# Kernel tuning notes

Measured on AMD Instinct MI355X. Metric: run time of the kernel, lower is better.

The kernel has to match this reference:

```python
import jax, jax.numpy as jnp
import numpy as np

N, DEG, F_IN, F_OUT, H = 8192, 16, 1024, 128, 8


def setup_inputs() -> dict:
    key = jax.random.key(0)
    ks = jax.random.split(key, 6)
    features = jax.random.normal(ks[0], (N, F_IN), dtype=jnp.float32)
    adj = jax.random.randint(ks[1], (N, DEG), 0, N)  # fixed-degree adjacency
    W = jax.random.normal(ks[2], (H, F_IN, F_OUT), dtype=jnp.float32) / np.sqrt(F_IN)
    bW = jax.random.normal(ks[3], (H, F_OUT), dtype=jnp.float32) * 0.01
    a = jax.random.normal(ks[4], (H, 2 * F_OUT), dtype=jnp.float32) / np.sqrt(2.0 * F_OUT)
    ba = jax.random.normal(ks[5], (H,), dtype=jnp.float32) * 0.01
    return {"features": features, "adj": adj, "W": W, "bW": bW, "a": a, "ba": ba}


def reference(features, adj, W, bW, a, ba):
    n = features.shape[0]
    # neighbors with self appended last (matches adjlist[node] + [node])
    nbr = jnp.concatenate([adj, jnp.arange(n)[:, None]], axis=1)  # [N, DEG+1]
    # per-head linear transform: h[k] = features @ W_k + b_k
    h = jnp.einsum('nf,hfo->hno', features, W) + bW[:, None, :]  # [H, N, F_OUT]
    # attention score a_k([h_dst, h_src]) + bias decomposed into dst/src parts
    a_dst, a_src = a[:, :F_OUT], a[:, F_OUT:]
    s_dst = jnp.einsum('hno,ho->hn', h, a_dst)  # [H, N]
    s_src = jnp.einsum('hno,ho->hn', h, a_src)  # [H, N]
    scores = s_dst[:, :, None] + s_src[:, nbr] + ba[:, None, None]  # [H, N, DEG+1]
    scores = jax.nn.leaky_relu(scores, 0.2)
    alpha = jax.nn.softmax(scores, axis=-1)  # softmax over neighbors (incl. self)
    h_src = h[:, nbr]  # [H, N, DEG+1, F_OUT]
    out = jnp.einsum('hnd,hndf->hnf', alpha, h_src)  # [H, N, F_OUT]
    # concat heads along feature dim -> [N, H*F_OUT]
    return out.transpose(1, 0, 2).reshape(n, H * F_OUT)
```

## Files before the change

### kernel.cpp

```cpp
#include <hip/hip_runtime.h>
#include <hip/hip_bf16.h>

#define N_NODES 8192
#define DEG     16
#define F_IN    1024
#define F_OUT   128
#define NH      8

typedef __bf16 bf16x8 __attribute__((ext_vector_type(8)));
typedef float  f32x4  __attribute__((ext_vector_type(4)));

__device__ __forceinline__ float bf2f(unsigned short u) {
    union { unsigned int i; float f; } v;
    v.i = ((unsigned int)u) << 16;
    return v.f;
}
__device__ __forceinline__ unsigned short f2bf(float f) {
    union { float f; unsigned int u; } v; v.f = f;
    unsigned int u = v.u + 0x7FFFu + ((v.u >> 16) & 1u);
    return (unsigned short)(u >> 16);
}
__device__ __forceinline__ int detect_bf16(const unsigned int* __restrict__ w) {
    int hits = 0;
#pragma unroll
    for (int i = 0; i < 64; ++i) {
        unsigned int x = w[i * 131 + 17];
        int e = (x >> 7) & 0xFF;
        hits += (e >= 100 && e <= 140) ? 1 : 0;
    }
    return hits > 32;
}
__device__ __forceinline__ float rd_scalar(const void* p, int idx, int isbf) {
    return isbf ? bf2f(((const unsigned short*)p)[idx]) : ((const float*)p)[idx];
}
__device__ __forceinline__ void gload16(const void* g, void* l) {
    __builtin_amdgcn_global_load_lds(
        (const __attribute__((address_space(1))) void*)g,
        (__attribute__((address_space(3))) void*)l, 16, 0, 0);
}

__global__ __launch_bounds__(256) void prep_inputs(
    const void* __restrict__ feat, const void* __restrict__ W,
    unsigned short* __restrict__ featb, unsigned short* __restrict__ Wt)
{
    const int isbf = detect_bf16((const unsigned int*)feat);
    if (blockIdx.x < 4096) {
        size_t i8 = ((size_t)blockIdx.x * 256 + threadIdx.x) * 8;
        if (isbf) {
            *(uint4*)(featb + i8) = ((const uint4*)feat)[i8 / 8];
        } else {
            const float* s = (const float*)feat + i8;
            float4 u0 = *(const float4*)s;
            float4 u1 = *(const float4*)(s + 4);
            unsigned short t[8] = { f2bf(u0.x), f2bf(u0.y), f2bf(u0.z), f2bf(u0.w),
                                    f2bf(u1.x), f2bf(u1.y), f2bf(u1.z), f2bf(u1.w) };
            *(uint4*)(featb + i8) = *(const uint4*)t;
        }
    } else {
        __shared__ float tile[64][65];
        const int bx = blockIdx.x - 4096;
        const int h  = bx >> 5;
        const int kt = (bx >> 1) & 15;
        const int ot = bx & 1;
        const int t  = threadIdx.x;
#pragma unroll
        for (int i = 0; i < 16; ++i) {
            int id = i * 256 + t, r = id >> 6, c = id & 63;
            tile[r][c] = rd_scalar(W, ((h * 1024 + kt * 64 + r) * 128) + ot * 64 + c, isbf);
        }
        __syncthreads();
#pragma unroll
        for (int i = 0; i < 16; ++i) {
            int id = i * 256 + t, oc = id >> 6, kc = id & 63;
            Wt[(size_t)(h * 128 + ot * 64 + oc) * 1024 + kt * 64 + kc] = f2bf(tile[kc][oc]);
        }
    }
}

__global__ __launch_bounds__(256) void gat_gemm3(
    const unsigned short* __restrict__ featb,
    const unsigned short* __restrict__ Wt,
    const void* __restrict__ raw_feat,
    const void* __restrict__ bW, const void* __restrict__ a,
    const void* __restrict__ ba,
    __hip_bfloat16* __restrict__ hbuf,
    float* __restrict__ sdst, float* __restrict__ ssrc)
{
    const int rawbf = detect_bf16((const unsigned int*)raw_feat);

    const int h   = blockIdx.y;
    const int bxp = ((blockIdx.x & 7) << 3) | (blockIdx.x >> 3);
    const int n0  = bxp * 128;
    const int tid = threadIdx.x;

    __shared__ __align__(16) unsigned short As[2][128 * 64];
    __shared__ __align__(16) unsigned short Bs[2][128 * 64];

    const int lane = tid & 63;
    const int wave = tid >> 6;
    const int quad = lane >> 4;
    const int l16  = lane & 15;
    const int sw   = l16 & 7;

    f32x4 acc[2][8];
#pragma unroll
    for (int i = 0; i < 2; ++i)
#pragma unroll
        for (int j = 0; j < 8; ++j) acc[i][j] = (f32x4)0.f;

    const unsigned short* wbase = Wt + (size_t)h * F_OUT * F_IN;

    for (int k0 = 0; k0 < F_IN; k0 += 128) {
#pragma unroll
        for (int p = 0; p < 2; ++p) {
            const int kk0 = k0 + p * 64;
#pragma unroll
            for (int t = 0; t < 4; ++t) {
                const int r0  = t * 32 + wave * 8;
                const int row = r0 + (lane >> 3);
                const int gc  = (lane & 7) ^ (row & 7);
                gload16(&featb[(size_t)(n0 + row) * F_IN + kk0 + gc * 8],
                        &As[p][r0 * 64]);
                gload16(&wbase[(size_t)row * F_IN + kk0 + gc * 8],
                        &Bs[p][r0 * 64]);
            }
        }
        __syncthreads();

#pragma unroll
        for (int p = 0; p < 2; ++p) {
#pragma unroll
            for (int ks = 0; ks < 2; ++ks) {
                const int kc = ks * 4 + quad;
                const int cs = (kc ^ sw) * 8;
                bf16x8 af[2], bfr[8];
#pragma unroll
                for (int rt = 0; rt < 2; ++rt)
                    af[rt] = *(const bf16x8*)&As[p][(wave * 32 + rt * 16 + l16) * 64 + cs];
#pragma unroll
                for (int ct = 0; ct < 8; ++ct)
                    bfr[ct] = *(const bf16x8*)&Bs[p][(ct * 16 + l16) * 64 + cs];
#pragma unroll
                for (int rt = 0; rt < 2; ++rt)
#pragma unroll
                    for (int ct = 0; ct < 8; ++ct)
                        acc[rt][ct] = __builtin_amdgcn_mfma_f32_16x16x32_bf16(
                            af[rt], bfr[ct], acc[rt][ct], 0, 0, 0);
            }
        }
        __syncthreads();
    }

#pragma unroll
    for (int ct = 0; ct < 8; ++ct) {
        const int col = ct * 16 + l16;
        const float bwv = rd_scalar(bW, h * F_OUT + col, rawbf);
#pragma unroll
        for (int rt = 0; rt < 2; ++rt) {
            const int nrow = n0 + wave * 32 + rt * 16 + quad * 4;
            __hip_bfloat16* dst = hbuf + ((size_t)h * N_NODES + nrow) * F_OUT + col;
#pragma unroll
            for (int r = 0; r < 4; ++r)
                dst[(size_t)r * F_OUT] = __float2bfloat16(acc[rt][ct][r] + bwv);
        }
    }

    float adst[8], asrc[8];
#pragma unroll
    for (int ct = 0; ct < 8; ++ct) {
        const int col = ct * 16 + l16;
        adst[ct] = rd_scalar(a, h * 256 + col, rawbf);
        asrc[ct] = rd_scalar(a, h * 256 + 128 + col, rawbf);
    }
    float pd[2][4] = {}, ps[2][4] = {};
#pragma unroll
    for (int rt = 0; rt < 2; ++rt)
#pragma unroll
        for (int ct = 0; ct < 8; ++ct)
#pragma unroll
            for (int r = 0; r < 4; ++r) {
                pd[rt][r] += acc[rt][ct][r] * adst[ct];
                ps[rt][r] += acc[rt][ct][r] * asrc[ct];
            }
#pragma unroll
    for (int off = 1; off < 16; off <<= 1)
#pragma unroll
        for (int rt = 0; rt < 2; ++rt)
#pragma unroll
            for (int r = 0; r < 4; ++r) {
                pd[rt][r] += __shfl_xor(pd[rt][r], off, 64);
                ps[rt][r] += __shfl_xor(ps[rt][r], off, 64);
            }
    if (l16 == 0) {
        const float bav = rd_scalar(ba, h, rawbf);
#pragma unroll
        for (int rt = 0; rt < 2; ++rt) {
            const int base = n0 + wave * 32 + rt * 16 + quad * 4;
            float4 vd = { pd[rt][0] + bav, pd[rt][1] + bav,
                          pd[rt][2] + bav, pd[rt][3] + bav };
            float4 vs = { ps[rt][0], ps[rt][1], ps[rt][2], ps[rt][3] };
            *(float4*)&sdst[h * N_NODES + base] = vd;
            *(float4*)&ssrc[h * N_NODES + base] = vs;
        }
    }
}

__global__ __launch_bounds__(256) void gat_aggr4(
    const unsigned short* __restrict__ hbuf,
    const int* __restrict__ adj,
    const float* __restrict__ sdst, const float* __restrict__ ssrc,
    const void* __restrict__ raw_feat, void* __restrict__ out)
{
    const int isbf = detect_bf16((const unsigned int*)raw_feat);
    const int h    = blockIdx.x;
    const int wave = threadIdx.x >> 6;
    const int lane = threadIdx.x & 63;
    const int half = lane >> 5;
    const int l32  = lane & 31;
    const int n    = blockIdx.y * 8 + wave * 2 + half;

    int nbr = n;
    if (l32 < DEG) nbr = adj[n * DEG + l32];

    float s = -1e30f;
    if (l32 < 17) {
        float sv = sdst[h * N_NODES + n] + ssrc[h * N_NODES + nbr];
        s = sv > 0.f ? sv : 0.2f * sv;
    }
    float m = s;
#pragma unroll
    for (int off = 1; off < 32; off <<= 1)
        m = fmaxf(m, __shfl_xor(m, off, 64));
    float ev = (l32 < 17) ? __expf(s - m) : 0.f;
    float sum = ev;
#pragma unroll
    for (int off = 1; off < 32; off <<= 1)
        sum += __shfl_xor(sum, off, 64);
    ev *= (1.f / sum);

    const unsigned short* hb = hbuf + (size_t)h * N_NODES * F_OUT;
    const int fc    = l32 * 4;
    const int sbase = half << 5;
    float a0 = 0.f, a1 = 0.f, a2 = 0.f, a3 = 0.f;
#pragma unroll
    for (int d = 0; d < 17; ++d) {
        const int   nb = __shfl(nbr, sbase + d, 64);
        const float av = __shfl(ev,  sbase + d, 64);
        uint2 pk = *(const uint2*)&hb[(size_t)nb * F_OUT + fc];
        a0 += av * bf2f((unsigned short)(pk.x & 0xffffu));
        a1 += av * bf2f((unsigned short)(pk.x >> 16));
        a2 += av * bf2f((unsigned short)(pk.y & 0xffffu));
        a3 += av * bf2f((unsigned short)(pk.y >> 16));
    }

    const size_t oidx = (size_t)n * (NH * F_OUT) + h * F_OUT + fc;
    if (isbf) {
        uint2 res;
        res.x = (unsigned int)f2bf(a0) | ((unsigned int)f2bf(a1) << 16);
        res.y = (unsigned int)f2bf(a2) | ((unsigned int)f2bf(a3) << 16);
        *(uint2*)&((unsigned short*)out)[oidx] = res;
    } else {
        float4 res = { a0, a1, a2, a3 };
        *(float4*)&((float*)out)[oidx] = res;
    }
}

__global__ __launch_bounds__(256) void gat_gemm_fb(
    const void* __restrict__ feat, const void* __restrict__ W,
    const void* __restrict__ bW, __hip_bfloat16* __restrict__ hbuf)
{
    const int isbf = detect_bf16((const unsigned int*)feat);
    const int h = blockIdx.y, n0 = blockIdx.x * 128, tid = threadIdx.x;
    __shared__ __align__(16) unsigned short As[128][72];
    __shared__ __align__(16) unsigned short Bs[128][72];
    const int lane = tid & 63, wave = tid >> 6, quad = lane >> 4, l16 = lane & 15;
    f32x4 acc[2][8];
#pragma unroll
    for (int i = 0; i < 2; ++i)
#pragma unroll
        for (int j = 0; j < 8; ++j) acc[i][j] = (f32x4)0.f;
    for (int k0 = 0; k0 < F_IN; k0 += 64) {
        if (isbf) {
            const unsigned short* fbase = (const unsigned short*)feat + (size_t)n0 * F_IN;
            const unsigned short* wsrc  = (const unsigned short*)W +
                                          (size_t)h * F_IN * F_OUT + (size_t)k0 * F_OUT;
#pragma unroll
            for (int t = 0; t < 4; ++t) {
                int c = t * 256 + tid, row = c >> 3, kc = c & 7;
                *(uint4*)&As[row][kc * 8] = *(const uint4*)&fbase[row * F_IN + k0 + kc * 8];
            }
#pragma unroll
            for (int t = 0; t < 2; ++t) {
                int c = t * 256 + tid, kr2 = c >> 4, mm = c & 15, oc = mm * 8;
                uint4 w0 = *(const uint4*)&wsrc[(2 * kr2) * F_OUT + oc];
                uint4 w1 = *(const uint4*)&wsrc[(2 * kr2 + 1) * F_OUT + oc];
                const unsigned short* p0 = (const unsigned short*)&w0;
                const unsigned short* p1 = (const unsigned short*)&w1;
#pragma unroll
                for (int j = 0; j < 8; ++j) {
                    int i = (j + mm) & 7;
                    *(unsigned int*)&Bs[oc + i][2 * kr2] =
                        (unsigned int)p0[i] | ((unsigned int)p1[i] << 16);
                }
            }
        } else {
            const float* fbase = (const float*)feat + (size_t)n0 * F_IN;
            const float* wsrc  = (const float*)W +
                                 (size_t)h * F_IN * F_OUT + (size_t)k0 * F_OUT;
#pragma unroll
            for (int t = 0; t < 4; ++t) {
                int c = t * 256 + tid, row = c >> 3, kc = c & 7;
                const float* src = &fbase[row * F_IN + k0 + kc * 8];
                float4 u0 = *(const float4*)src, u1 = *(const float4*)(src + 4);
                unsigned short sh[8] = { f2bf(u0.x), f2bf(u0.y), f2bf(u0.z), f2bf(u0.w),
                                         f2bf(u1.x), f2bf(u1.y), f2bf(u1.z), f2bf(u1.w) };
                *(uint4*)&As[row][kc * 8] = *(const uint4*)sh;
            }
#pragma unroll
            for (int t = 0; t < 2; ++t) {
                int c = t * 256 + tid, kr2 = c >> 4, mm = c & 15, oc = mm * 8;
                const float* r0 = &wsrc[(2 * kr2) * F_OUT + oc];
                const float* r1 = &wsrc[(2 * kr2 + 1) * F_OUT + oc];
                float4 e0 = *(const float4*)r0, e1 = *(const float4*)(r0 + 4);
                float4 o0 = *(const float4*)r1, o1 = *(const float4*)(r1 + 4);
                unsigned short p0[8] = { f2bf(e0.x), f2bf(e0.y), f2bf(e0.z), f2bf(e0.w),
                                         f2bf(e1.x), f2bf(e1.y), f2bf(e1.z), f2bf(e1.w) };
                unsigned short p1[8] = { f2bf(o0.x), f2bf(o0.y), f2bf(o0.z), f2bf(o0.w),
                                         f2bf(o1.x), f2bf(o1.y), f2bf(o1.z), f2bf(o1.w) };
#pragma unroll
                for (int j = 0; j < 8; ++j) {
                    int i = (j + mm) & 7;
                    *(unsigned int*)&Bs[oc + i][2 * kr2] =
                        (unsigned int)p0[i] | ((unsigned int)p1[i] << 16);
                }
            }
        }
        __syncthreads();
#pragma unroll
        for (int ks = 0; ks < 2; ++ks) {
            const int kk = ks * 32 + quad * 8;
            bf16x8 af[2], bfr[8];
#pragma unroll
            for (int rt = 0; rt < 2; ++rt)
                af[rt] = *(const bf16x8*)&As[wave * 32 + rt * 16 + l16][kk];
#pragma unroll
            for (int ct = 0; ct < 8; ++ct)
                bfr[ct] = *(const bf16x8*)&Bs[ct * 16 + l16][kk];
#pragma unroll
            for (int rt = 0; rt < 2; ++rt)
#pragma unroll
                for (int ct = 0; ct < 8; ++ct)
                    acc[rt][ct] = __builtin_amdgcn_mfma_f32_16x16x32_bf16(
                        af[rt], bfr[ct], acc[rt][ct], 0, 0, 0);
        }
        __syncthreads();
    }
#pragma unroll
    for (int ct = 0; ct < 8; ++ct) {
        const int col = ct * 16 + l16;
        const float bwv = rd_scalar(bW, h * F_OUT + col, isbf);
#pragma unroll
        for (int rt = 0; rt < 2; ++rt) {
            const int nrow = n0 + wave * 32 + rt * 16 + quad * 4;
            __hip_bfloat16* dst = hbuf + ((size_t)h * N_NODES + nrow) * F_OUT + col;
#pragma unroll
            for (int r = 0; r < 4; ++r)
                dst[(size_t)r * F_OUT] = __float2bfloat16(acc[rt][ct][r] + bwv);
        }
    }
}

__global__ __launch_bounds__(256) void gat_aggr_fb(
    const __hip_bfloat16* __restrict__ hbuf, const int* __restrict__ adj,
    const void* __restrict__ a, const void* __restrict__ ba,
    void* __restrict__ out, const void* __restrict__ feat)
{
    const int isbf = detect_bf16((const unsigned int*)feat);
    const int n = blockIdx.x, wave = threadIdx.x >> 6, lane = threadIdx.x & 63;
    const int hh = blockIdx.y * 4 + wave;
    int nbr_reg = n;
    if (lane < DEG) nbr_reg = adj[n * DEG + lane];
    const int f0 = lane * 2;
    const float adst0 = rd_scalar(a, hh * 256 + f0, isbf);
    const float adst1 = rd_scalar(a, hh * 256 + f0 + 1, isbf);
    const float asrc0 = rd_scalar(a, hh * 256 + 128 + f0, isbf);
    const float asrc1 = rd_scalar(a, hh * 256 + 128 + f0 + 1, isbf);
    const float bav   = rd_scalar(ba, hh, isbf);
    const __hip_bfloat16* hb = hbuf + (size_t)hh * N_NODES * F_OUT;
    float v0[17], v1[17], red[18];
#pragma unroll
    for (int d = 0; d < 17; ++d) {
        int nb = __shfl(nbr_reg, d, 64);
        unsigned int pk = *(const unsigned int*)&hb[(size_t)nb * F_OUT + f0];
        v0[d] = bf2f((unsigned short)(pk & 0xffffu));
        v1[d] = bf2f((unsigned short)(pk >> 16));
        red[d] = v0[d] * asrc0 + v1[d] * asrc1;
    }
    red[17] = v0[16] * adst0 + v1[16] * adst1;
#pragma unroll
    for (int off = 1; off < 64; off <<= 1)
#pragma unroll
        for (int r = 0; r < 18; ++r) red[r] += __shfl_xor(red[r], off, 64);
    const float sd = red[17] + bav;
    float sc[17], mx = -1e30f;
#pragma unroll
    for (int d = 0; d < 17; ++d) {
        float s = sd + red[d];
        s = s > 0.f ? s : 0.2f * s;
        sc[d] = s; mx = fmaxf(mx, s);
    }
    float ssum = 0.f;
#pragma unroll
    for (int d = 0; d < 17; ++d) { sc[d] = __expf(sc[d] - mx); ssum += sc[d]; }
    const float inv = 1.f / ssum;
    float o0 = 0.f, o1 = 0.f;
#pragma unroll
    for (int d = 0; d < 17; ++d) { o0 += sc[d] * v0[d]; o1 += sc[d] * v1[d]; }
    o0 *= inv; o1 *= inv;
    const size_t oidx = (size_t)n * (NH * F_OUT) + hh * F_OUT + f0;
    if (isbf) {
        *(unsigned int*)&((unsigned short*)out)[oidx] =
            (unsigned int)f2bf(o0) | ((unsigned int)f2bf(o1) << 16);
    } else {
        float2 res; res.x = o0; res.y = o1;
        *(float2*)&((float*)out)[oidx] = res;
    }
}

extern "C" void kernel_launch(void* const* d_in, const int* in_sizes, int n_in,
                              void* d_out, int out_size, void* d_ws, size_t ws_size,
                              hipStream_t stream)
{
    const void* feat = d_in[0];
    const int*  adj  = (const int*)d_in[1];
    const void* W    = d_in[2];
    const void* bW   = d_in[3];
    const void* a    = d_in[4];
    const void* ba   = d_in[5];

    char* ws = (char*)d_ws;
    __hip_bfloat16* hbuf = (__hip_bfloat16*)ws;
    const size_t HB = (size_t)NH * N_NODES * F_OUT * 2;
    const size_t SC = (size_t)NH * N_NODES * 4;
    float* sdst = (float*)(ws + HB);
    float* ssrc = (float*)(ws + HB + SC);
    unsigned short* featb = (unsigned short*)(ws + HB + 2 * SC);
    unsigned short* Wt    = featb + (size_t)N_NODES * F_IN;
    const size_t needA = HB + 2 * SC +
        ((size_t)N_NODES * F_IN + (size_t)NH * F_IN * F_OUT) * 2;

    if (ws_size >= needA) {
        prep_inputs<<<4352, 256, 0, stream>>>(feat, W, featb, Wt);
        gat_gemm3<<<dim3(64, 8), 256, 0, stream>>>(featb, Wt, feat, bW, a, ba,
                                                   hbuf, sdst, ssrc);
        gat_aggr4<<<dim3(8, 1024), 256, 0, stream>>>((const unsigned short*)hbuf,
                                                     adj, sdst, ssrc, feat, d_out);
    } else {
        gat_gemm_fb<<<dim3(64, 8), 256, 0, stream>>>(feat, W, bW, hbuf);
        gat_aggr_fb<<<dim3(8192, 2), 256, 0, stream>>>(hbuf, adj, a, ba, d_out, feat);
    }
}
```

Baseline: 148.7 us.

## Split GEMM block across 8 waves in a 4x2 grid with LDS score reduction

The projection GEMM now runs with 512 threads per block, arranged as a 4x2 wave grid, so each wave computes a 32x64 output subtile instead of 32x128. This halves the accumulator registers per wave and doubles the waves available to hide latency, with each wave issuing fewer global loads per stage. Because the attention-score dot products are now split across two column waves, the partial sums are combined through shared memory, which adds a block barrier. The cost is more LDS fragment reads per MFMA, since the A fragments are loaded by two waves, and a little extra synchronisation.

```diff
diff --git a/kernel.cpp b/kernel.cpp
--- a/kernel.cpp
+++ b/kernel.cpp
@@ -77,7 +77,7 @@
     }
 }
 
-__global__ __launch_bounds__(256) void gat_gemm3(
+__global__ __launch_bounds__(512, 4) void gat_gemm6(
     const unsigned short* __restrict__ featb,
     const unsigned short* __restrict__ Wt,
     const void* __restrict__ raw_feat,
@@ -98,15 +98,19 @@
 
     const int lane = tid & 63;
     const int wave = tid >> 6;
+    const int wr   = wave >> 1;
+    const int wc   = wave & 1;
     const int quad = lane >> 4;
     const int l16  = lane & 15;
     const int sw   = l16 & 7;
-
-    f32x4 acc[2][8];
+    const int srow   = lane >> 3;
+    const int schunk = lane & 7;
+
+    f32x4 acc[2][4];
 #pragma unroll
     for (int i = 0; i < 2; ++i)
 #pragma unroll
-        for (int j = 0; j < 8; ++j) acc[i][j] = (f32x4)0.f;
+        for (int j = 0; j < 4; ++j) acc[i][j] = (f32x4)0.f;
 
     const unsigned short* wbase = Wt + (size_t)h * F_OUT * F_IN;
 
@@ -115,10 +119,10 @@
         for (int p = 0; p < 2; ++p) {
             const int kk0 = k0 + p * 64;
 #pragma unroll
-            for (int t = 0; t < 4; ++t) {
-                const int r0  = t * 32 + wave * 8;
-                const int row = r0 + (lane >> 3);
-                const int gc  = (lane & 7) ^ (row & 7);
+            for (int t = 0; t < 2; ++t) {
+                const int r0  = t * 64 + wave * 8;
+                const int row = r0 + srow;
+                const int gc  = schunk ^ (row & 7);
                 gload16(&featb[(size_t)(n0 + row) * F_IN + kk0 + gc * 8],
                         &As[p][r0 * 64]);
                 gload16(&wbase[(size_t)row * F_IN + kk0 + gc * 8],
@@ -133,17 +137,17 @@
             for (int ks = 0; ks < 2; ++ks) {
                 const int kc = ks * 4 + quad;
                 const int cs = (kc ^ sw) * 8;
-                bf16x8 af[2], bfr[8];
+                bf16x8 af[2], bfr[4];
 #pragma unroll
                 for (int rt = 0; rt < 2; ++rt)
-                    af[rt] = *(const bf16x8*)&As[p][(wave * 32 + rt * 16 + l16) * 64 + cs];
-#pragma unroll
-                for (int ct = 0; ct < 8; ++ct)
-                    bfr[ct] = *(const bf16x8*)&Bs[p][(ct * 16 + l16) * 64 + cs];
+                    af[rt] = *(const bf16x8*)&As[p][(wr * 32 + rt * 16 + l16) * 64 + cs];
+#pragma unroll
+                for (int ct = 0; ct < 4; ++ct)
+                    bfr[ct] = *(const bf16x8*)&Bs[p][(wc * 64 + ct * 16 + l16) * 64 + cs];
 #pragma unroll
                 for (int rt = 0; rt < 2; ++rt)
 #pragma unroll
-                    for (int ct = 0; ct < 8; ++ct)
+                    for (int ct = 0; ct < 4; ++ct)
                         acc[rt][ct] = __builtin_amdgcn_mfma_f32_16x16x32_bf16(
                             af[rt], bfr[ct], acc[rt][ct], 0, 0, 0);
             }
@@ -152,12 +156,12 @@
     }
 
 #pragma unroll
-    for (int ct = 0; ct < 8; ++ct) {
-        const int col = ct * 16 + l16;
+    for (int ct = 0; ct < 4; ++ct) {
+        const int col = wc * 64 + ct * 16 + l16;
         const float bwv = rd_scalar(bW, h * F_OUT + col, rawbf);
 #pragma unroll
         for (int rt = 0; rt < 2; ++rt) {
-            const int nrow = n0 + wave * 32 + rt * 16 + quad * 4;
+            const int nrow = n0 + wr * 32 + rt * 16 + quad * 4;
             __hip_bfloat16* dst = hbuf + ((size_t)h * N_NODES + nrow) * F_OUT + col;
 #pragma unroll
             for (int r = 0; r < 4; ++r)
@@ -165,10 +169,10 @@
         }
     }
 
-    float adst[8], asrc[8];
-#pragma unroll
-    for (int ct = 0; ct < 8; ++ct) {
-        const int col = ct * 16 + l16;
+    float adst[4], asrc[4];
+#pragma unroll
+    for (int ct = 0; ct < 4; ++ct) {
+        const int col = wc * 64 + ct * 16 + l16;
         adst[ct] = rd_scalar(a, h * 256 + col, rawbf);
         asrc[ct] = rd_scalar(a, h * 256 + 128 + col, rawbf);
     }
@@ -176,7 +180,7 @@
 #pragma unroll
     for (int rt = 0; rt < 2; ++rt)
 #pragma unroll
-        for (int ct = 0; ct < 8; ++ct)
+        for (int ct = 0; ct < 4; ++ct)
 #pragma unroll
             for (int r = 0; r < 4; ++r) {
                 pd[rt][r] += acc[rt][ct][r] * adst[ct];
@@ -191,17 +195,28 @@
                 pd[rt][r] += __shfl_xor(pd[rt][r], off, 64);
                 ps[rt][r] += __shfl_xor(ps[rt][r], off, 64);
             }
+
+    float* sred = (float*)&As[0][0];
     if (l16 == 0) {
+#pragma unroll
+        for (int rt = 0; rt < 2; ++rt)
+#pragma unroll
+            for (int r = 0; r < 4; ++r) {
+                const int row32 = rt * 16 + quad * 4 + r;
+                sred[((wr * 2 + wc) * 2 + 0) * 32 + row32] = pd[rt][r];
+                sred[((wr * 2 + wc) * 2 + 1) * 32 + row32] = ps[rt][r];
+            }
+    }
+    __syncthreads();
+    if (wc == 0 && lane < 32) {
         const float bav = rd_scalar(ba, h, rawbf);
-#pragma unroll
-        for (int rt = 0; rt < 2; ++rt) {
-            const int base = n0 + wave * 32 + rt * 16 + quad * 4;
-            float4 vd = { pd[rt][0] + bav, pd[rt][1] + bav,
-                          pd[rt][2] + bav, pd[rt][3] + bav };
-            float4 vs = { ps[rt][0], ps[rt][1], ps[rt][2], ps[rt][3] };
-            *(float4*)&sdst[h * N_NODES + base] = vd;
-            *(float4*)&ssrc[h * N_NODES + base] = vs;
-        }
+        const float vd = sred[((wr * 2 + 0) * 2 + 0) * 32 + lane]
+                       + sred[((wr * 2 + 1) * 2 + 0) * 32 + lane] + bav;
+        const float vs = sred[((wr * 2 + 0) * 2 + 1) * 32 + lane]
+                       + sred[((wr * 2 + 1) * 2 + 1) * 32 + lane];
+        const int nrow = n0 + wr * 32 + lane;
+        sdst[h * N_NODES + nrow] = vd;
+        ssrc[h * N_NODES + nrow] = vs;
     }
 }
 
@@ -451,7 +466,7 @@
 
     if (ws_size >= needA) {
         prep_inputs<<<4352, 256, 0, stream>>>(feat, W, featb, Wt);
-        gat_gemm3<<<dim3(64, 8), 256, 0, stream>>>(featb, Wt, feat, bW, a, ba,
+        gat_gemm6<<<dim3(64, 8), 512, 0, stream>>>(featb, Wt, feat, bW, a, ba,
                                                    hbuf, sdst, ssrc);
         gat_aggr4<<<dim3(8, 1024), 256, 0, stream>>>((const unsigned short*)hbuf,
                                                      adj, sdst, ssrc, feat, d_out);
```

Result: no change. 148.1 us (-0.4%).
